# Optimization experiments

Measured on AMD Instinct MI355X. Metric: run time of the kernel, lower is better.

Reference implementation:

```python
import jax, jax.numpy as jnp
import numpy as np

PAD_ID, CLS_ID, SEP_ID = 0, 101, 102
B, S, D = 16, 1024, 1024
SOFTMAX_THRESHOLD = 1e-3


def setup_inputs() -> dict:
    key = jax.random.key(0)
    k1, k2, k3, k4 = jax.random.split(key, 4)
    h_src = jax.random.normal(k1, (B, S, D), dtype=jnp.float32)
    h_tgt = jax.random.normal(k2, (B, S, D), dtype=jnp.float32)
    ids_src = jax.random.randint(k3, (B, S), 103, 30000)
    ids_tgt = jax.random.randint(k4, (B, S), 103, 30000)
    # realistic token structure: CLS at 0, trailing PAD with SEP before it
    ids_src = ids_src.at[:, 0].set(CLS_ID).at[:, S - 64:].set(PAD_ID).at[:, S - 65].set(SEP_ID)
    ids_tgt = ids_tgt.at[:, 0].set(CLS_ID).at[:, S - 128:].set(PAD_ID).at[:, S - 129].set(SEP_ID)
    return {"hidden_states_src": h_src, "hidden_states_tgt": h_tgt,
            "inputs_src": ids_src, "inputs_tgt": ids_tgt}


def _special_mask(ids):
    # 1.0 at pad/cls/sep positions (positions excluded from alignment)
    return ((ids == PAD_ID) | (ids == CLS_ID) | (ids == SEP_ID)).astype(jnp.float32)


def reference(hidden_states_src, hidden_states_tgt, inputs_src, inputs_tgt):
    m_src = _special_mask(inputs_src)            # [B,Ss]
    m_tgt = _special_mask(inputs_tgt)            # [B,St]
    len_src = jnp.sum(1.0 - m_src, axis=-1)      # [B]
    len_tgt = jnp.sum(1.0 - m_tgt, axis=-1)      # [B]
    # (1 - (1 - mask)) * -10000 == mask * -10000
    add_src = m_src * -10000.0                   # [B,Ss]
    add_tgt = m_tgt * -10000.0                   # [B,St]

    # single-head QK^T scores [B,Ss,St]
    scores = jnp.einsum('bsd,btd->bst', hidden_states_src, hidden_states_tgt)
    scores_src = scores + add_tgt[:, None, :]    # mask tgt cols, softmax over t
    scores_tgt = scores + add_src[:, :, None]    # mask src rows, softmax over s

    probs_src = jax.nn.softmax(scores_src, axis=-1)
    probs_tgt = jax.nn.softmax(scores_tgt, axis=-2)
    align_matrix = (probs_src > SOFTMAX_THRESHOLD) & (probs_tgt > SOFTMAX_THRESHOLD)

    # length-temperature softmaxes for output probabilities
    p_src = jax.nn.softmax(scores_src / jnp.sqrt(len_tgt)[:, None, None], axis=-1)
    p_tgt = jax.nn.softmax(scores_tgt / jnp.sqrt(len_src)[:, None, None], axis=-2)
    align_prob = 2.0 * p_src * p_tgt / (p_src + p_tgt + 1e-9)

    # re-add singleton head dim to match torch output shape [B,1,Ss,St]
    return align_matrix[:, None], align_prob[:, None]
```

## Files before the change

### kernel.cpp

```cpp
#include <hip/hip_runtime.h>
#include <math.h>
#include <stdint.h>

#define NB 16
#define SQ 1024
#define DD 1024

typedef _Float16 f16x8 __attribute__((ext_vector_type(8)));
typedef float f32x4 __attribute__((ext_vector_type(4)));

__global__ void prep_kernel(const int* __restrict__ ids_src, const int* __restrict__ ids_tgt,
                            float* __restrict__ add_src, float* __restrict__ add_tgt,
                            float* __restrict__ itau){
  int b = blockIdx.x;
  __shared__ int csrc, ctgt;
  if (threadIdx.x == 0){ csrc = 0; ctgt = 0; }
  __syncthreads();
  int ls = 0, lt = 0;
  for (int i = threadIdx.x; i < SQ; i += blockDim.x){
    int id = ids_src[b*SQ + i];
    bool sp = (id == 0) || (id == 101) || (id == 102);
    add_src[b*SQ + i] = sp ? -10000.0f : 0.0f;
    ls += sp ? 0 : 1;
    id = ids_tgt[b*SQ + i];
    sp = (id == 0) || (id == 101) || (id == 102);
    add_tgt[b*SQ + i] = sp ? -10000.0f : 0.0f;
    lt += sp ? 0 : 1;
  }
  atomicAdd(&csrc, ls);
  atomicAdd(&ctgt, lt);
  __syncthreads();
  if (threadIdx.x == 0){
    itau[b]      = 1.0f / sqrtf((float)csrc);
    itau[NB + b] = 1.0f / sqrtf((float)ctgt);
  }
}

#define NKS 32

__global__ __launch_bounds__(256, 2)
void gemm_fsplit(const float* __restrict__ A, const float* __restrict__ Bm,
                 float* __restrict__ C,
                 const float* __restrict__ add_src, const float* __restrict__ add_tgt,
                 const float* __restrict__ itau,
                 float* __restrict__ rpart, float* __restrict__ cpart){
  __shared__ _Float16 lds[2][4][128*32];
  const int tid  = threadIdx.x;
  const int wave = tid >> 6;
  const int lane = tid & 63;

  int bid = blockIdx.x;
  int wg  = (bid & 7) * 128 + (bid >> 3);
  int b   = wg >> 6;
  int by  = (wg >> 3) & 7;
  int bx  = wg & 7;

  const float* Ab = A  + ((size_t)b*SQ + by*128) * DD;
  const float* Bb = Bm + ((size_t)b*SQ + bx*128) * DD;

  const int sr = tid >> 2;
  const int ss = tid & 3;
  const int wsl = ss ^ ((sr >> 1) & 3);
  const int w0 = (sr      *4 + wsl)*8;
  const int w1 = ((sr+64) *4 + wsl)*8;

  float4 rg[4][2];
  auto LOADR = [&](int k0){
    const float* pa0 = Ab + (size_t)sr*DD      + k0 + ss*8;
    const float* pa1 = Ab + (size_t)(sr+64)*DD + k0 + ss*8;
    const float* pb0 = Bb + (size_t)sr*DD      + k0 + ss*8;
    const float* pb1 = Bb + (size_t)(sr+64)*DD + k0 + ss*8;
    rg[0][0] = *(const float4*)pa0; rg[0][1] = *(const float4*)(pa0+4);
    rg[1][0] = *(const float4*)pa1; rg[1][1] = *(const float4*)(pa1+4);
    rg[2][0] = *(const float4*)pb0; rg[2][1] = *(const float4*)(pb0+4);
    rg[3][0] = *(const float4*)pb1; rg[3][1] = *(const float4*)(pb1+4);
  };
  auto WRITE = [&](int bu){
    #pragma unroll
    for (int u = 0; u < 4; ++u){
      const float* v = (const float*)&rg[u][0];
      f16x8 h, l;
      #pragma unroll
      for (int j = 0; j < 8; ++j){
        _Float16 hh = (_Float16)v[j];
        h[j] = hh;
        l[j] = (_Float16)((v[j] - (float)hh) * 4096.0f);
      }
      const int hp = (u < 2) ? 0 : 2;
      const int wo = (u & 1) ? w1 : w0;
      *(f16x8*)&lds[bu][hp  ][wo] = h;
      *(f16x8*)&lds[bu][hp+1][wo] = l;
    }
  };

  const int lr  = lane & 15;
  const int ls8 = (((lane >> 4) ^ ((lr >> 1) & 3)) << 3);
  const int wm  = (wave >> 1) * 64;
  const int wn  = (wave & 1) * 64;
  const int aoffL = (wm + lr)*32 + ls8;
  const int boffL = (wn + lr)*32 + ls8;

  f32x4 accm[4][4], accc[4][4];
  #pragma unroll
  for (int m = 0; m < 4; ++m)
    #pragma unroll
    for (int n = 0; n < 4; ++n){ accm[m][n] = (f32x4)0.0f; accc[m][n] = (f32x4)0.0f; }

  LOADR(0);
  WRITE(0);
  __syncthreads();

  for (int t = 0; t < NKS; ++t){
    const int bu = t & 1;
    if (t + 1 < NKS) LOADR((t+1)*32);

    f16x8 ah[4], al[4], bh[4], bl[4];
    #pragma unroll
    for (int m = 0; m < 4; ++m){
      ah[m] = *(const f16x8*)&lds[bu][0][aoffL + m*512];
      al[m] = *(const f16x8*)&lds[bu][1][aoffL + m*512];
      bh[m] = *(const f16x8*)&lds[bu][2][boffL + m*512];
      bl[m] = *(const f16x8*)&lds[bu][3][boffL + m*512];
    }
    #pragma unroll
    for (int m = 0; m < 4; ++m)
      #pragma unroll
      for (int n = 0; n < 4; ++n){
        accm[m][n] = __builtin_amdgcn_mfma_f32_16x16x32_f16(ah[m], bh[n], accm[m][n], 0, 0, 0);
        accc[m][n] = __builtin_amdgcn_mfma_f32_16x16x32_f16(ah[m], bl[n], accc[m][n], 0, 0, 0);
        accc[m][n] = __builtin_amdgcn_mfma_f32_16x16x32_f16(al[m], bh[n], accc[m][n], 0, 0, 0);
      }

    if (t + 1 < NKS) WRITE(bu ^ 1);
    __syncthreads();
  }

  const float inv = 1.0f / 4096.0f;
  const int r0 = (lane >> 4) * 4;
  const int c0 = lane & 15;

  float* Cb = C + ((size_t)b*SQ + by*128 + wm)*SQ + bx*128 + wn;
  #pragma unroll
  for (int m = 0; m < 4; ++m)
    #pragma unroll
    for (int n = 0; n < 4; ++n)
      #pragma unroll
      for (int j = 0; j < 4; ++j)
        Cb[(size_t)(m*16 + r0 + j)*SQ + n*16 + c0] = fmaf(accc[m][n][j], inv, accm[m][n][j]);

  const float its = itau[b];
  const float itt = itau[NB + b];
  float at4[4];
  #pragma unroll
  for (int n = 0; n < 4; ++n)
    at4[n] = add_tgt[b*SQ + bx*128 + wn + n*16 + c0];

  {
    size_t rb = ((size_t)(b*16 + bx*2 + (wave & 1)))*3*SQ + by*128 + wm;
    #pragma unroll
    for (int m = 0; m < 4; ++m){
      float mx[4], s1[4], s2[4];
      #pragma unroll
      for (int j = 0; j < 4; ++j){
        float v = -1e30f;
        #pragma unroll
        for (int n = 0; n < 4; ++n)
          v = fmaxf(v, fmaf(accc[m][n][j], inv, accm[m][n][j]) + at4[n]);
        #pragma unroll
        for (int o = 1; o < 16; o <<= 1) v = fmaxf(v, __shfl_xor(v, o));
        mx[j] = v;
      }
      #pragma unroll
      for (int j = 0; j < 4; ++j){
        float a = 0.f, c = 0.f;
        #pragma unroll
        for (int n = 0; n < 4; ++n){
          float d = fmaf(accc[m][n][j], inv, accm[m][n][j]) + at4[n] - mx[j];
          a += expf(d);
          c += expf(d * itt);
        }
        #pragma unroll
        for (int o = 1; o < 16; o <<= 1){ a += __shfl_xor(a, o); c += __shfl_xor(c, o); }
        s1[j] = a; s2[j] = c;
      }
      if ((lane & 15) == 0){
        #pragma unroll
        for (int j = 0; j < 4; ++j){
          int rr = m*16 + r0 + j;
          rpart[rb + rr]        = mx[j];
          rpart[rb + SQ + rr]   = s1[j];
          rpart[rb + 2*SQ + rr] = s2[j];
        }
      }
    }
  }

  {
    float asv[4][4];
    #pragma unroll
    for (int m = 0; m < 4; ++m)
      #pragma unroll
      for (int j = 0; j < 4; ++j)
        asv[m][j] = add_src[b*SQ + by*128 + wm + m*16 + r0 + j];

    size_t cb2 = ((size_t)(b*16 + by*2 + (wave >> 1)))*3*SQ + bx*128 + wn;
    #pragma unroll
    for (int n = 0; n < 4; ++n){
      float mx = -1e30f;
      #pragma unroll
      for (int m = 0; m < 4; ++m)
        #pragma unroll
        for (int j = 0; j < 4; ++j)
          mx = fmaxf(mx, fmaf(accc[m][n][j], inv, accm[m][n][j]) + asv[m][j]);
      mx = fmaxf(mx, __shfl_xor(mx, 16));
      mx = fmaxf(mx, __shfl_xor(mx, 32));
      float s1 = 0.f, s2 = 0.f;
      #pragma unroll
      for (int m = 0; m < 4; ++m)
        #pragma unroll
        for (int j = 0; j < 4; ++j){
          float d = fmaf(accc[m][n][j], inv, accm[m][n][j]) + asv[m][j] - mx;
          s1 += expf(d);
          s2 += expf(d * its);
        }
      s1 += __shfl_xor(s1, 16); s1 += __shfl_xor(s1, 32);
      s2 += __shfl_xor(s2, 16); s2 += __shfl_xor(s2, 32);
      if (lane < 16){
        int cc = n*16 + c0;
        cpart[cb2 + cc]        = mx;
        cpart[cb2 + SQ + cc]   = s1;
        cpart[cb2 + 2*SQ + cc] = s2;
      }
    }
  }
}

__global__ void merge_stats(const float* __restrict__ rpart, const float* __restrict__ cpart,
                            const float* __restrict__ itau,
                            float* __restrict__ Mr, float* __restrict__ S1r, float* __restrict__ S2r,
                            float* __restrict__ Mc, float* __restrict__ S1c, float* __restrict__ S2c){
  int idx = blockIdx.x*256 + threadIdx.x;
  int b = idx >> 10;
  int pos = idx & 1023;
  const float* P = blockIdx.y ? cpart : rpart;
  float it = blockIdx.y ? itau[b] : itau[NB + b];
  float M = -1e30f;
  #pragma unroll 4
  for (int ch = 0; ch < 16; ++ch)
    M = fmaxf(M, P[((size_t)(b*16 + ch))*3*SQ + pos]);
  float s1 = 0.f, s2 = 0.f;
  #pragma unroll 4
  for (int ch = 0; ch < 16; ++ch){
    size_t base = ((size_t)(b*16 + ch))*3*SQ + pos;
    float mm = P[base];
    s1 += P[base + SQ]   * expf(mm - M);
    s2 += P[base + 2*SQ] * expf((mm - M)*it);
  }
  if (blockIdx.y == 0){ Mr[idx] = M; S1r[idx] = s1; S2r[idx] = s2; }
  else                { Mc[idx] = M; S1c[idx] = s1; S2c[idx] = s2; }
}

__global__ __launch_bounds__(256)
void gemm_nt(const float* __restrict__ A, const float* __restrict__ Bm, float* __restrict__ C){
  __shared__ float As[32][132];
  __shared__ float Bs[32][132];
  const int b = blockIdx.z;
  const float* Ab = A  + ((size_t)b*SQ + blockIdx.y*128) * DD;
  const float* Bb = Bm + ((size_t)b*SQ + blockIdx.x*128) * DD;
  const int tid = threadIdx.x;
  const int lr = tid >> 3;
  const int lc = (tid & 7) << 2;
  const int tx = tid & 15;
  const int ty = tid >> 4;

  float acc[8][8];
  #pragma unroll
  for (int i = 0; i < 8; ++i)
    #pragma unroll
    for (int j = 0; j < 8; ++j) acc[i][j] = 0.0f;

  for (int k0 = 0; k0 < DD; k0 += 32){
    #pragma unroll
    for (int p = 0; p < 4; ++p){
      int row = p*32 + lr;
      float4 va = *(const float4*)(Ab + (size_t)row*DD + k0 + lc);
      float4 vb = *(const float4*)(Bb + (size_t)row*DD + k0 + lc);
      As[lc+0][row] = va.x; As[lc+1][row] = va.y; As[lc+2][row] = va.z; As[lc+3][row] = va.w;
      Bs[lc+0][row] = vb.x; Bs[lc+1][row] = vb.y; Bs[lc+2][row] = vb.z; Bs[lc+3][row] = vb.w;
    }
    __syncthreads();
    #pragma unroll
    for (int k = 0; k < 32; ++k){
      float a[8], bb[8];
      *(float4*)(a)    = *(const float4*)&As[k][ty*4];
      *(float4*)(a+4)  = *(const float4*)&As[k][64 + ty*4];
      *(float4*)(bb)   = *(const float4*)&Bs[k][tx*4];
      *(float4*)(bb+4) = *(const float4*)&Bs[k][64 + tx*4];
      #pragma unroll
      for (int i = 0; i < 8; ++i)
        #pragma unroll
        for (int j = 0; j < 8; ++j)
          acc[i][j] = fmaf(a[i], bb[j], acc[i][j]);
    }
    __syncthreads();
  }

  float* Cb = C + (size_t)b*SQ*SQ + (size_t)(blockIdx.y*128)*SQ + blockIdx.x*128;
  #pragma unroll
  for (int i = 0; i < 8; ++i){
    int r = (i < 4) ? (ty*4 + i) : (64 + ty*4 + (i-4));
    *(float4*)(Cb + (size_t)r*SQ + tx*4)      = make_float4(acc[i][0],acc[i][1],acc[i][2],acc[i][3]);
    *(float4*)(Cb + (size_t)r*SQ + 64 + tx*4) = make_float4(acc[i][4],acc[i][5],acc[i][6],acc[i][7]);
  }
}

#define NCH 64
__global__ __launch_bounds__(256)
void stats_pass(const float* __restrict__ scores,
                const float* __restrict__ add_src, const float* __restrict__ add_tgt,
                const float* __restrict__ itau,
                float* __restrict__ Mr, float* __restrict__ S1r, float* __restrict__ S2r,
                float* __restrict__ part){
  __shared__ float redm[16][4];
  __shared__ float red1[16][4];
  __shared__ float red2[16][4];
  const int b  = blockIdx.x >> 6;
  const int ch = blockIdx.x & 63;
  const int tid = threadIdx.x;
  const int wv = tid >> 6;
  const int t0 = tid << 2;
  const float its = itau[b];
  const float itt = itau[NB + b];

  const float* p = scores + ((size_t)b*SQ + ch*16)*SQ + t0;
  float4 at4 = *(const float4*)(add_tgt + b*SQ + t0);

  float4 x[16];
  #pragma unroll
  for (int s = 0; s < 16; ++s) x[s] = *(const float4*)(p + (size_t)s*SQ);

  #pragma unroll
  for (int s = 0; s < 16; ++s){
    float m = fmaxf(fmaxf(x[s].x + at4.x, x[s].y + at4.y),
                    fmaxf(x[s].z + at4.z, x[s].w + at4.w));
    #pragma unroll
    for (int o = 32; o > 0; o >>= 1) m = fmaxf(m, __shfl_xor(m, o));
    if ((tid & 63) == 0) redm[s][wv] = m;
  }
  __syncthreads();
  float Mrow[16];
  #pragma unroll
  for (int s = 0; s < 16; ++s)
    Mrow[s] = fmaxf(fmaxf(redm[s][0], redm[s][1]), fmaxf(redm[s][2], redm[s][3]));

  #pragma unroll
  for (int s = 0; s < 16; ++s){
    float d0 = x[s].x + at4.x - Mrow[s];
    float d1 = x[s].y + at4.y - Mrow[s];
    float d2 = x[s].z + at4.z - Mrow[s];
    float d3 = x[s].w + at4.w - Mrow[s];
    float s1 = expf(d0) + expf(d1) + expf(d2) + expf(d3);
    float s2 = expf(d0*itt) + expf(d1*itt) + expf(d2*itt) + expf(d3*itt);
    #pragma unroll
    for (int o = 32; o > 0; o >>= 1){ s1 += __shfl_xor(s1, o); s2 += __shfl_xor(s2, o); }
    if ((tid & 63) == 0){ red1[s][wv] = s1; red2[s][wv] = s2; }
  }
  __syncthreads();
  if (tid < 16){
    int s = tid;
    int row = b*SQ + ch*16 + s;
    Mr[row]  = fmaxf(fmaxf(redm[s][0], redm[s][1]), fmaxf(redm[s][2], redm[s][3]));
    S1r[row] = red1[s][0] + red1[s][1] + red1[s][2] + red1[s][3];
    S2r[row] = red2[s][0] + red2[s][1] + red2[s][2] + red2[s][3];
  }

  float asv[16];
  #pragma unroll
  for (int s = 0; s < 16; ++s) asv[s] = add_src[b*SQ + ch*16 + s];

  float cm0 = -1e30f, cm1 = -1e30f, cm2 = -1e30f, cm3 = -1e30f;
  #pragma unroll
  for (int s = 0; s < 16; ++s){
    cm0 = fmaxf(cm0, x[s].x + asv[s]);
    cm1 = fmaxf(cm1, x[s].y + asv[s]);
    cm2 = fmaxf(cm2, x[s].z + asv[s]);
    cm3 = fmaxf(cm3, x[s].w + asv[s]);
  }
  float c10 = 0.f, c11 = 0.f, c12 = 0.f, c13 = 0.f;
  float c20 = 0.f, c21 = 0.f, c22 = 0.f, c23 = 0.f;
  #pragma unroll
  for (int s = 0; s < 16; ++s){
    float d0 = x[s].x + asv[s] - cm0;
    float d1 = x[s].y + asv[s] - cm1;
    float d2 = x[s].z + asv[s] - cm2;
    float d3 = x[s].w + asv[s] - cm3;
    c10 += expf(d0); c11 += expf(d1); c12 += expf(d2); c13 += expf(d3);
    c20 += expf(d0*its); c21 += expf(d1*its); c22 += expf(d2*its); c23 += expf(d3*its);
  }
  size_t base = (size_t)blockIdx.x * 3 * SQ + t0;
  *(float4*)(part + base)        = make_float4(cm0, cm1, cm2, cm3);
  *(float4*)(part + base + SQ)   = make_float4(c10, c11, c12, c13);
  *(float4*)(part + base + 2*SQ) = make_float4(c20, c21, c22, c23);
}

__global__ void col_merge(const float* __restrict__ part, const float* __restrict__ itau,
                          float* __restrict__ Mc, float* __restrict__ S1c, float* __restrict__ S2c){
  int idx = blockIdx.x*256 + threadIdx.x;
  int b = idx >> 10;
  int t = idx & 1023;
  float it = itau[b];
  float M = -1e30f;
  for (int ch = 0; ch < NCH; ++ch)
    M = fmaxf(M, part[(size_t)(b*NCH+ch)*3*SQ + t]);
  float s1 = 0.f, s2 = 0.f;
  for (int ch = 0; ch < NCH; ++ch){
    size_t base = (size_t)(b*NCH+ch)*3*SQ + t;
    float mm = part[base];
    s1 += part[base +   SQ] * expf(mm - M);
    s2 += part[base + 2*SQ] * expf((mm - M)*it);
  }
  Mc[idx] = M; S1c[idx] = s1; S2c[idx] = s2;
}

__global__ __launch_bounds__(256)
void finalize(const float* __restrict__ scores,
              const float* __restrict__ add_src, const float* __restrict__ add_tgt,
              const float* __restrict__ itau,
              const float* __restrict__ Mr, const float* __restrict__ S1r, const float* __restrict__ S2r,
              const float* __restrict__ Mc, const float* __restrict__ S1c, const float* __restrict__ S2c,
              float* __restrict__ out0, float* __restrict__ out1){
  int row = blockIdx.x;
  int b = row >> 10;
  float Mrv = Mr[row], s1r = S1r[row], s2r = S2r[row];
  float ads = add_src[row];
  float itt = itau[NB + b], its = itau[b];
  int t = threadIdx.x << 2;
  size_t off = (size_t)row*SQ + t;
  float4 x4  = *(const float4*)(scores + off);
  int bt = b*SQ + t;
  float4 at4 = *(const float4*)(add_tgt + bt);
  float4 mc4 = *(const float4*)(Mc  + bt);
  float4 c14 = *(const float4*)(S1c + bt);
  float4 c24 = *(const float4*)(S2c + bt);
  const float* xp  = (const float*)&x4;
  const float* atp = (const float*)&at4;
  const float* mcp = (const float*)&mc4;
  const float* c1p = (const float*)&c14;
  const float* c2p = (const float*)&c24;
  float o0[4], o1[4];
  #pragma unroll
  for (int j = 0; j < 4; ++j){
    float x  = xp[j];
    float xs = x + atp[j];
    float ps = expf(xs - Mrv) / s1r;
    float qs = expf((xs - Mrv)*itt) / s2r;
    float xt = x + ads;
    float pt = expf(xt - mcp[j]) / c1p[j];
    float qt = expf((xt - mcp[j])*its) / c2p[j];
    o0[j] = (ps > 1e-3f && pt > 1e-3f) ? 1.0f : 0.0f;
    o1[j] = 2.0f*qs*qt / (qs + qt + 1e-9f);
  }
  *(float4*)(out0 + off) = make_float4(o0[0],o0[1],o0[2],o0[3]);
  *(float4*)(out1 + off) = make_float4(o1[0],o1[1],o1[2],o1[3]);
}

extern "C" void kernel_launch(void* const* d_in, const int* in_sizes, int n_in,
                              void* d_out, int out_size, void* d_ws, size_t ws_size,
                              hipStream_t stream){
  const float* hsrc = (const float*)d_in[0];
  const float* htgt = (const float*)d_in[1];
  const int*   isrc = (const int*)d_in[2];
  const int*   itgt = (const int*)d_in[3];

  float* out0 = (float*)d_out;
  float* out1 = out0 + (size_t)NB*SQ*SQ;
  float* W = (float*)d_ws;

  const size_t NSQ2 = (size_t)NB*SQ*SQ;
  const size_t need_fast = (NSQ2 + 16384*2 + 32 + 6*NB*SQ + 2*(size_t)NB*16*3*SQ) * 4;

  if (ws_size >= need_fast){
    float* scores  = W;
    float* add_src = W + NSQ2;
    float* add_tgt = add_src + NB*SQ;
    float* itau    = add_tgt + NB*SQ;
    float* Mr      = itau + 32;
    float* S1r     = Mr  + NB*SQ;
    float* S2r     = S1r + NB*SQ;
    float* Mc      = S2r + NB*SQ;
    float* S1c     = Mc  + NB*SQ;
    float* S2c     = S1c + NB*SQ;
    float* rpart   = S2c + NB*SQ;
    float* cpart   = rpart + (size_t)NB*16*3*SQ;

    prep_kernel<<<NB, 256, 0, stream>>>(isrc, itgt, add_src, add_tgt, itau);
    gemm_fsplit<<<1024, 256, 0, stream>>>(hsrc, htgt, scores, add_src, add_tgt, itau,
                                          rpart, cpart);
    merge_stats<<<dim3(NB*SQ/256, 2), 256, 0, stream>>>(rpart, cpart, itau,
                                                        Mr, S1r, S2r, Mc, S1c, S2c);
    finalize<<<NB*SQ, 256, 0, stream>>>(scores, add_src, add_tgt, itau,
                                        Mr, S1r, S2r, Mc, S1c, S2c, out0, out1);
  } else {
    float* scores  = out1;
    float* add_src = W;
    float* add_tgt = W + 16384;
    float* itau    = W + 32768;
    float* Mr      = W + 32800;
    float* S1r     = Mr  + NB*SQ;
    float* S2r     = S1r + NB*SQ;
    float* Mc      = S2r + NB*SQ;
    float* S1c     = Mc  + NB*SQ;
    float* S2c     = S1c + NB*SQ;
    float* part    = S2c + NB*SQ;

    prep_kernel<<<NB, 256, 0, stream>>>(isrc, itgt, add_src, add_tgt, itau);
    gemm_nt<<<dim3(8, 8, NB), 256, 0, stream>>>(hsrc, htgt, scores);
    stats_pass<<<NB*NCH, 256, 0, stream>>>(scores, add_src, add_tgt, itau, Mr, S1r, S2r, part);
    col_merge<<<NB*SQ/256, 256, 0, stream>>>(part, itau, Mc, S1c, S2c);
    finalize<<<NB*SQ, 256, 0, stream>>>(scores, add_src, add_tgt, itau,
                                        Mr, S1r, S2r, Mc, S1c, S2c, out0, out1);
  }
}
```

Measured before the change: 224.6 us.

## Deepen GEMM prefetch to two register stages and use fast exp intrinsics

The split-fp16 MFMA GEMM main loop is unrolled by two with two register buffers. Global loads now run two k-steps ahead of the MFMA work, and LDS writes of the next tile are interleaved between compute phases, to hide more global-memory latency. All expf calls in the stats, merge and output kernels are also replaced with __expf to cut transcendental cost. The extra register buffer raises register pressure, and __expf may change threshold decisions near 1e-3.

```diff
diff --git a/kernel.cpp b/kernel.cpp
--- a/kernel.cpp
+++ b/kernel.cpp
@@ -64,8 +64,7 @@
   const int w0 = (sr      *4 + wsl)*8;
   const int w1 = ((sr+64) *4 + wsl)*8;
 
-  float4 rg[4][2];
-  auto LOADR = [&](int k0){
+  auto LOADR = [&](float4 (&rg)[4][2], int k0){
     const float* pa0 = Ab + (size_t)sr*DD      + k0 + ss*8;
     const float* pa1 = Ab + (size_t)(sr+64)*DD + k0 + ss*8;
     const float* pb0 = Bb + (size_t)sr*DD      + k0 + ss*8;
@@ -75,7 +74,7 @@
     rg[2][0] = *(const float4*)pb0; rg[2][1] = *(const float4*)(pb0+4);
     rg[3][0] = *(const float4*)pb1; rg[3][1] = *(const float4*)(pb1+4);
   };
-  auto WRITE = [&](int bu){
+  auto WRITE = [&](int bu, float4 (&rg)[4][2]){
     #pragma unroll
     for (int u = 0; u < 4; ++u){
       const float* v = (const float*)&rg[u][0];
@@ -106,14 +105,7 @@
     #pragma unroll
     for (int n = 0; n < 4; ++n){ accm[m][n] = (f32x4)0.0f; accc[m][n] = (f32x4)0.0f; }
 
-  LOADR(0);
-  WRITE(0);
-  __syncthreads();
-
-  for (int t = 0; t < NKS; ++t){
-    const int bu = t & 1;
-    if (t + 1 < NKS) LOADR((t+1)*32);
-
+  auto MFMA_TILE = [&](int bu){
     f16x8 ah[4], al[4], bh[4], bl[4];
     #pragma unroll
     for (int m = 0; m < 4; ++m){
@@ -130,8 +122,22 @@
         accc[m][n] = __builtin_amdgcn_mfma_f32_16x16x32_f16(ah[m], bl[n], accc[m][n], 0, 0, 0);
         accc[m][n] = __builtin_amdgcn_mfma_f32_16x16x32_f16(al[m], bh[n], accc[m][n], 0, 0, 0);
       }
-
-    if (t + 1 < NKS) WRITE(bu ^ 1);
+  };
+
+  float4 rgA[4][2], rgB[4][2];
+  LOADR(rgA, 0);
+  WRITE(0, rgA);
+  LOADR(rgB, 32);
+  __syncthreads();
+
+  for (int t = 0; t < NKS; t += 2){
+    if (t + 2 < NKS) LOADR(rgA, (t+2)*32);
+    MFMA_TILE(0);
+    WRITE(1, rgB);
+    __syncthreads();
+    if (t + 3 < NKS) LOADR(rgB, (t+3)*32);
+    MFMA_TILE(1);
+    if (t + 2 < NKS) WRITE(0, rgA);
     __syncthreads();
   }
 
@@ -176,8 +182,8 @@
         #pragma unroll
         for (int n = 0; n < 4; ++n){
           float d = fmaf(accc[m][n][j], inv, accm[m][n][j]) + at4[n] - mx[j];
-          a += expf(d);
-          c += expf(d * itt);
+          a += __expf(d);
+          c += __expf(d * itt);
         }
         #pragma unroll
         for (int o = 1; o < 16; o <<= 1){ a += __shfl_xor(a, o); c += __shfl_xor(c, o); }
@@ -220,8 +226,8 @@
         #pragma unroll
         for (int j = 0; j < 4; ++j){
           float d = fmaf(accc[m][n][j], inv, accm[m][n][j]) + asv[m][j] - mx;
-          s1 += expf(d);
-          s2 += expf(d * its);
+          s1 += __expf(d);
+          s2 += __expf(d * its);
         }
       s1 += __shfl_xor(s1, 16); s1 += __shfl_xor(s1, 32);
       s2 += __shfl_xor(s2, 16); s2 += __shfl_xor(s2, 32);
@@ -253,8 +259,8 @@
   for (int ch = 0; ch < 16; ++ch){
     size_t base = ((size_t)(b*16 + ch))*3*SQ + pos;
     float mm = P[base];
-    s1 += P[base + SQ]   * expf(mm - M);
-    s2 += P[base + 2*SQ] * expf((mm - M)*it);
+    s1 += P[base + SQ]   * __expf(mm - M);
+    s2 += P[base + 2*SQ] * __expf((mm - M)*it);
   }
   if (blockIdx.y == 0){ Mr[idx] = M; S1r[idx] = s1; S2r[idx] = s2; }
   else                { Mc[idx] = M; S1c[idx] = s1; S2c[idx] = s2; }
@@ -452,11 +458,11 @@
   for (int j = 0; j < 4; ++j){
     float x  = xp[j];
     float xs = x + atp[j];
-    float ps = expf(xs - Mrv) / s1r;
-    float qs = expf((xs - Mrv)*itt) / s2r;
+    float ps = __expf(xs - Mrv) / s1r;
+    float qs = __expf((xs - Mrv)*itt) / s2r;
     float xt = x + ads;
-    float pt = expf(xt - mcp[j]) / c1p[j];
-    float qt = expf((xt - mcp[j])*its) / c2p[j];
+    float pt = __expf(xt - mcp[j]) / c1p[j];
+    float qt = __expf((xt - mcp[j])*its) / c2p[j];
     o0[j] = (ps > 1e-3f && pt > 1e-3f) ? 1.0f : 0.0f;
     o1[j] = 2.0f*qs*qt / (qs + qt + 1e-9f);
   }
```

New measurement: 288.4 us. 28.4% more time.
